# Performance work log

Hardware: AMD Instinct MI355X
Metric: run time of the kernel (lower is better)

Reference implementation:

```python
import jax, jax.numpy as jnp
import numpy as np

B, N, C = 1, 512, 64
CONTEXT = 3
HIDDEN = 256
N_OUT = 1
N_FEAT = C * 2 * CONTEXT  # join='cat' -> 2*C, then context shifts triple it
EPS = 1e-5


def pairing_cat(x_l, x_r, context):
    b, n, c = x_l.shape
    xl = jnp.broadcast_to(x_l[:, :, None, :], (b, n, n, c))
    xr = jnp.broadcast_to(x_r[:, None, :, :], (b, n, n, c))
    x = jnp.concatenate((xl, xr), axis=3)  # [B,N,N,2C]
    if context > 1:
        z = [x]
        for d in range(1, context // 2 + 1):
            z_u = jnp.zeros_like(x).at[:, d:, :-d, :].set(x[:, :-d, d:, :])
            z_d = jnp.zeros_like(x).at[:, :-d, d:, :].set(x[:, d:, :-d, :])
            z.append(z_u)
            z.append(z_d)
        x = jnp.concatenate(z, axis=3)  # [B,N,N,2C*context]
    return x


def setup_inputs() -> dict:
    key = jax.random.key(0)
    k = jax.random.split(key, 8)
    s1 = 1.0 / np.sqrt(N_FEAT)
    s2 = 1.0 / np.sqrt(HIDDEN)
    return {
        "x_l": jax.random.normal(k[0], (B, N, C), dtype=jnp.float32),
        "x_r": jax.random.normal(k[1], (B, N, C), dtype=jnp.float32),
        "W1": jax.random.uniform(k[2], (N_FEAT, HIDDEN), jnp.float32, -s1, s1),
        "b1": jax.random.uniform(k[3], (HIDDEN,), jnp.float32, -s1, s1),
        "gamma": jnp.ones((HIDDEN,), jnp.float32),
        "beta": jnp.zeros((HIDDEN,), jnp.float32),
        "W2": jax.random.uniform(k[4], (HIDDEN, N_OUT), jnp.float32, -s2, s2),
        "b2": jax.random.uniform(k[5], (N_OUT,), jnp.float32, -s2, s2),
    }


def reference(x_l, x_r, W1, b1, gamma, beta, W2, b2):
    x = pairing_cat(x_l, x_r, CONTEXT)  # [B,N,N,N_FEAT]
    h = jnp.einsum('bijf,fh->bijh', x, W1) + b1
    mu = jnp.mean(h, axis=-1, keepdims=True)
    var = jnp.mean(jnp.square(h - mu), axis=-1, keepdims=True)
    h = (h - mu) * jax.lax.rsqrt(var + EPS) * gamma + beta
    h = jax.nn.celu(h)  # dropout_rate=0.0 -> identity in eval/train
    y = jnp.einsum('bijh,ho->bijo', h, W2) + b2
    return y  # [B,N,N,1]
```

## Files before the change

### kernel.cpp

```cpp
#include <hip/hip_runtime.h>
#include <hip/hip_bf16.h>

#define NN  512
#define CC  64
#define HID 256
#define H4  (HID/4)
#define PSTRIDE (NN*HID)
#define PROWS 2

typedef short  bf16x8 __attribute__((ext_vector_type(8)));
typedef float  f32x4  __attribute__((ext_vector_type(4)));

__global__ __launch_bounds__(256) void proj_kernel(
    const float* __restrict__ xl, const float* __restrict__ xr,
    const float* __restrict__ W1, const float* __restrict__ b1,
    float* __restrict__ P)
{
  const int side = blockIdx.y;
  const int i0   = blockIdx.x * PROWS;
  const int h    = threadIdx.x;
  const float* __restrict__ x = side ? xr : xl;

  __shared__ float xs[PROWS][CC];
  if (threadIdx.x < PROWS * CC)
    xs[threadIdx.x >> 6][threadIdx.x & 63] = x[i0 * CC + threadIdx.x];
  __syncthreads();

  float acc0[PROWS], acc1[PROWS], acc2[PROWS];
#pragma unroll
  for (int r = 0; r < PROWS; r++) { acc0[r] = 0.f; acc1[r] = 0.f; acc2[r] = 0.f; }

  const int base = side ? CC : 0;
  const float* __restrict__ w0p = W1 + (base      ) * HID + h;
  const float* __restrict__ w1p = W1 + (base + 128) * HID + h;
  const float* __restrict__ w2p = W1 + (base + 256) * HID + h;
#pragma unroll 8
  for (int c = 0; c < CC; c++) {
    float w0 = w0p[c * HID];
    float w1 = w1p[c * HID];
    float w2 = w2p[c * HID];
#pragma unroll
    for (int r = 0; r < PROWS; r++) {
      float xv = xs[r][c];
      acc0[r] = fmaf(xv, w0, acc0[r]);
      acc1[r] = fmaf(xv, w1, acc1[r]);
      acc2[r] = fmaf(xv, w2, acc2[r]);
    }
  }

  float* __restrict__ O0 = P + (side ? 3 : 0) * PSTRIDE;
  float* __restrict__ O1 = P + (side ? 4 : 1) * PSTRIDE;
  float* __restrict__ O2 = P + (side ? 5 : 2) * PSTRIDE;
  const float bb = side ? 0.f : b1[h];
#pragma unroll
  for (int r = 0; r < PROWS; r++) {
    O0[(i0 + r) * HID + h] = acc0[r] + bb;
    O1[(i0 + r) * HID + h] = acc1[r];
    O2[(i0 + r) * HID + h] = acc2[r];
  }
}

__global__ __launch_bounds__(256) void prep_kernel(
    const float* __restrict__ P,
    float* __restrict__ Uf, float* __restrict__ Vf,
    unsigned short* __restrict__ Ubf, unsigned short* __restrict__ Vbf,
    float* __restrict__ rowstat)
{
  const int r = blockIdx.x, h = threadIdx.x;
  const float* __restrict__ PA = P;
  const float* __restrict__ PC = P + 1 * PSTRIDE;
  const float* __restrict__ PE = P + 2 * PSTRIDE;
  const float* __restrict__ PB = P + 3 * PSTRIDE;
  const float* __restrict__ PD = P + 4 * PSTRIDE;
  const float* __restrict__ PF = P + 5 * PSTRIDE;

  float u = PA[r * HID + h] + PC[(r - 1) * HID + h] + PE[(r + 1) * HID + h];
  float v = PB[r * HID + h] + PD[(r + 1) * HID + h] + PF[(r - 1) * HID + h];
  Uf[r * HID + h] = u;
  Vf[r * HID + h] = v;
  __hip_bfloat16 ub = __float2bfloat16(u), vb = __float2bfloat16(v);
  Ubf[r * HID + h] = *(unsigned short*)&ub;
  Vbf[r * HID + h] = *(unsigned short*)&vb;

  float u2 = u * u, v2 = v * v;
#pragma unroll
  for (int k = 32; k >= 1; k >>= 1) {
    u  += __shfl_xor(u,  k, 64);
    u2 += __shfl_xor(u2, k, 64);
    v  += __shfl_xor(v,  k, 64);
    v2 += __shfl_xor(v2, k, 64);
  }
  __shared__ float red[4][4];
  const int w = h >> 6;
  if ((h & 63) == 0) { red[w][0] = u; red[w][1] = u2; red[w][2] = v; red[w][3] = v2; }
  __syncthreads();
  if (h < 4)
    rowstat[h * NN + r] = red[0][h] + red[1][h] + red[2][h] + red[3][h];
}

__global__ __launch_bounds__(256) void cross_kernel(
    const unsigned short* __restrict__ Ubf,
    const unsigned short* __restrict__ Vbf,
    float* __restrict__ Cross)
{
  const int wave = threadIdx.x >> 6, lane = threadIdx.x & 63;
  const int t  = blockIdx.x * 4 + wave;
  const int ti = t >> 5, tj = t & 31;
  const int i0 = ti * 16, j0 = tj * 16;
  const int rc = lane & 15, kb = (lane >> 4) * 8;

  f32x4 acc = {0.f, 0.f, 0.f, 0.f};
#pragma unroll
  for (int k = 0; k < HID; k += 32) {
    bf16x8 a = *(const bf16x8*)(Ubf + (size_t)(i0 + rc) * HID + k + kb);
    bf16x8 b = *(const bf16x8*)(Vbf + (size_t)(j0 + rc) * HID + k + kb);
    acc = __builtin_amdgcn_mfma_f32_16x16x32_bf16(a, b, acc, 0, 0, 0);
  }
  const int orow = (lane >> 4) * 4, ocol = lane & 15;
#pragma unroll
  for (int r = 0; r < 4; r++)
    Cross[(size_t)(i0 + orow + r) * NN + j0 + ocol] = acc[r];
}

__device__ __forceinline__ float celu1(float x) {
  return fmaxf(x, 0.f) + fminf(__expf(x) - 1.f, 0.f);
}

__global__ __launch_bounds__(256) void pair_kernel(
    const float* __restrict__ P,
    const float* __restrict__ Uf, const float* __restrict__ Vf,
    const float* __restrict__ Cross, const float* __restrict__ rowstat,
    const float* __restrict__ gamma, const float* __restrict__ beta,
    const float* __restrict__ W2, const float* __restrict__ b2,
    float* __restrict__ out)
{
  const int wave = threadIdx.x >> 6, lane = threadIdx.x & 63;
  const float b2s = b2[0];

  if (blockIdx.x < 2040) {
    const int i     = 1 + (blockIdx.x >> 2);
    const int chunk = blockIdx.x & 3;
    const int g = lane >> 4, q = lane & 15;

    const float4* U4 = (const float4*)(Uf + i * HID + q * 16);
    const float4 u0 = U4[0], u1 = U4[1], u2 = U4[2], u3 = U4[3];
    const float4* G4 = (const float4*)(gamma + q * 16);
    const float4 ga0 = G4[0], ga1 = G4[1], ga2 = G4[2], ga3 = G4[3];
    const float4* B4 = (const float4*)(beta + q * 16);
    const float4 bt0 = B4[0], bt1 = B4[1], bt2 = B4[2], bt3 = B4[3];
    const float4* W4 = (const float4*)(W2 + q * 16);
    const float4 w0 = W4[0], w1 = W4[1], w2 = W4[2], w3 = W4[3];

    const float sUi  = rowstat[0 * NN + i];
    const float sU2i = rowstat[1 * NN + i];
    const float* __restrict__ sV  = rowstat + 2 * NN;
    const float* __restrict__ sV2 = rowstat + 3 * NN;

    const int jbase = 1 + chunk * 128 + wave * 32 + g;
    for (int m = 0; m < 8; m++) {
      const int j  = jbase + m * 4;
      const int jc = j <= 510 ? j : 510;
      const float4* V4 = (const float4*)(Vf + jc * HID + q * 16);
      const float4 v0 = V4[0], v1 = V4[1], v2 = V4[2], v3 = V4[3];
      const float Cr = Cross[i * NN + jc];
      const float mu = (sUi + sV[jc]) * (1.f / HID);
      const float t  = fmaf(2.f, Cr, sU2i + sV2[jc]) * (1.f / HID);
      const float rs = rsqrtf(t - mu * mu + 1e-5f);
      const float mrs = -mu * rs;

      float racc = 0.f;
      auto doh = [&](float U, float V, float G, float Bt, float W) {
        float s = U + V;
        float z = fmaf(s, rs, mrs);
        float n = fmaf(z, G, Bt);
        racc = fmaf(celu1(n), W, racc);
      };
      doh(u0.x, v0.x, ga0.x, bt0.x, w0.x);
      doh(u0.y, v0.y, ga0.y, bt0.y, w0.y);
      doh(u0.z, v0.z, ga0.z, bt0.z, w0.z);
      doh(u0.w, v0.w, ga0.w, bt0.w, w0.w);
      doh(u1.x, v1.x, ga1.x, bt1.x, w1.x);
      doh(u1.y, v1.y, ga1.y, bt1.y, w1.y);
      doh(u1.z, v1.z, ga1.z, bt1.z, w1.z);
      doh(u1.w, v1.w, ga1.w, bt1.w, w1.w);
      doh(u2.x, v2.x, ga2.x, bt2.x, w2.x);
      doh(u2.y, v2.y, ga2.y, bt2.y, w2.y);
      doh(u2.z, v2.z, ga2.z, bt2.z, w2.z);
      doh(u2.w, v2.w, ga2.w, bt2.w, w2.w);
      doh(u3.x, v3.x, ga3.x, bt3.x, w3.x);
      doh(u3.y, v3.y, ga3.y, bt3.y, w3.y);
      doh(u3.z, v3.z, ga3.z, bt3.z, w3.z);
      doh(u3.w, v3.w, ga3.w, bt3.w, w3.w);

#pragma unroll
      for (int k = 1; k <= 8; k <<= 1)
        racc += __shfl_xor(racc, k, 64);
      if (q == 0 && j <= 510)
        out[i * NN + j] = racc + b2s;
    }
  } else {
    const int gw = (blockIdx.x - 2040) * 4 + wave;
    const float4* P4 = (const float4*)P;
    const float4* PA = P4 + 0 * (PSTRIDE / 4);
    const float4* PC = P4 + 1 * (PSTRIDE / 4);
    const float4* PE = P4 + 2 * (PSTRIDE / 4);
    const float4* PB = P4 + 3 * (PSTRIDE / 4);
    const float4* PD = P4 + 4 * (PSTRIDE / 4);
    const float4* PF = P4 + 5 * (PSTRIDE / 4);
    const float4 g  = ((const float4*)gamma)[lane];
    const float4 be = ((const float4*)beta)[lane];
    const float4 w2 = ((const float4*)W2)[lane];

    for (int tt = 0; tt < 16; tt++) {
      const int p = gw * 16 + tt;
      if (p >= 2044) break;
      int i, j;
      if      (p < 512)  { i = 0;        j = p;        }
      else if (p < 1024) { i = 511;      j = p - 512;  }
      else if (p < 1534) { i = p - 1023; j = 0;        }
      else               { i = p - 1533; j = 511;      }

      const float4 a  = PA[i * H4 + lane];
      const float4 cu = PC[(i - 1) * H4 + lane];
      const float4 ed = PE[(i + 1) * H4 + lane];
      const float4 b  = PB[j * H4 + lane];
      const float4 du = PD[(j + 1) * H4 + lane];
      const float4 fd = PF[(j - 1) * H4 + lane];
      const float mu_m = (i >= 1 && j <= NN - 2) ? 1.f : 0.f;
      const float md_m = (i <= NN - 2 && j >= 1) ? 1.f : 0.f;

      float s0 = fmaf(md_m, ed.x + fd.x, fmaf(mu_m, cu.x + du.x, a.x + b.x));
      float s1 = fmaf(md_m, ed.y + fd.y, fmaf(mu_m, cu.y + du.y, a.y + b.y));
      float s2 = fmaf(md_m, ed.z + fd.z, fmaf(mu_m, cu.z + du.z, a.z + b.z));
      float s3 = fmaf(md_m, ed.w + fd.w, fmaf(mu_m, cu.w + du.w, a.w + b.w));

      float sum = (s0 + s1) + (s2 + s3);
      float ssq = fmaf(s0, s0, fmaf(s1, s1, fmaf(s2, s2, s3 * s3)));
#pragma unroll
      for (int off = 32; off >= 1; off >>= 1) {
        sum += __shfl_xor(sum, off, 64);
        ssq += __shfl_xor(ssq, off, 64);
      }
      const float mu  = sum * (1.f / HID);
      const float var = fmaf(ssq, 1.f / HID, -mu * mu);
      const float rs  = rsqrtf(var + 1e-5f);
      const float mrs = -mu * rs;

      auto nrm = [&](float s, float G, float Bt) {
        return fmaf(fmaf(s, rs, mrs), G, Bt);
      };
      float racc = fmaf(celu1(nrm(s0, g.x, be.x)), w2.x,
                   fmaf(celu1(nrm(s1, g.y, be.y)), w2.y,
                   fmaf(celu1(nrm(s2, g.z, be.z)), w2.z,
                        celu1(nrm(s3, g.w, be.w)) * w2.w)));
#pragma unroll
      for (int off = 32; off >= 1; off >>= 1)
        racc += __shfl_xor(racc, off, 64);
      if (lane == 0) out[i * NN + j] = racc + b2s;
    }
  }
}

extern "C" void kernel_launch(void* const* d_in, const int* in_sizes, int n_in,
                              void* d_out, int out_size, void* d_ws, size_t ws_size,
                              hipStream_t stream)
{
  const float* xl    = (const float*)d_in[0];
  const float* xr    = (const float*)d_in[1];
  const float* W1    = (const float*)d_in[2];
  const float* b1    = (const float*)d_in[3];
  const float* gamma = (const float*)d_in[4];
  const float* beta  = (const float*)d_in[5];
  const float* W2    = (const float*)d_in[6];
  const float* b2    = (const float*)d_in[7];
  float* out = (float*)d_out;

  float* P     = (float*)d_ws;
  float* Uf    = P + 6 * PSTRIDE;
  float* Vf    = Uf + NN * HID;
  float* Cross = Vf + NN * HID;
  unsigned short* Ubf = (unsigned short*)(Cross + NN * NN);
  unsigned short* Vbf = Ubf + NN * HID;
  float* rowstat = (float*)(Vbf + NN * HID);

  proj_kernel<<<dim3(NN / PROWS, 2), 256, 0, stream>>>(xl, xr, W1, b1, P);
  prep_kernel<<<NN, 256, 0, stream>>>(P, Uf, Vf, Ubf, Vbf, rowstat);
  cross_kernel<<<256, 256, 0, stream>>>(Ubf, Vbf, Cross);
  pair_kernel<<<2040 + 32, 256, 0, stream>>>(P, Uf, Vf, Cross, rowstat,
                                             gamma, beta, W2, b2, out);
}
```

Baseline: 124.5 us.

## Rebalance border work across more blocks, schedule first; split accumulators in pair kernel

The border-pair work moves from 32 trailing blocks of 16 pairs per wave to 256 leading blocks of 2 pairs per wave. This is meant to stop the slow border tail from running after the interior blocks finish. The interior loop now uses four independent accumulators to shorten the FMA dependency chain, simplifies CELU to a select, unrolls by 2, and adds an occupancy hint to launch bounds. The extra unrolling and the occupancy target may raise register pressure.

```diff
diff --git a/kernel.cpp b/kernel.cpp
--- a/kernel.cpp
+++ b/kernel.cpp
@@ -7,6 +7,7 @@
 #define H4  (HID/4)
 #define PSTRIDE (NN*HID)
 #define PROWS 2
+#define NB_BORDER 256
 
 typedef short  bf16x8 __attribute__((ext_vector_type(8)));
 typedef float  f32x4  __attribute__((ext_vector_type(4)));
@@ -123,10 +124,11 @@
 }
 
 __device__ __forceinline__ float celu1(float x) {
-  return fmaxf(x, 0.f) + fminf(__expf(x) - 1.f, 0.f);
-}
-
-__global__ __launch_bounds__(256) void pair_kernel(
+  float e = __expf(x) - 1.f;
+  return x > 0.f ? x : e;
+}
+
+__global__ __launch_bounds__(256, 6) void pair_kernel(
     const float* __restrict__ P,
     const float* __restrict__ Uf, const float* __restrict__ Vf,
     const float* __restrict__ Cross, const float* __restrict__ rowstat,
@@ -137,9 +139,10 @@
   const int wave = threadIdx.x >> 6, lane = threadIdx.x & 63;
   const float b2s = b2[0];
 
-  if (blockIdx.x < 2040) {
-    const int i     = 1 + (blockIdx.x >> 2);
-    const int chunk = blockIdx.x & 3;
+  if (blockIdx.x >= NB_BORDER) {
+    const int bx    = blockIdx.x - NB_BORDER;
+    const int i     = 1 + (bx >> 2);
+    const int chunk = bx & 3;
     const int g = lane >> 4, q = lane & 15;
 
     const float4* U4 = (const float4*)(Uf + i * HID + q * 16);
@@ -157,6 +160,7 @@
     const float* __restrict__ sV2 = rowstat + 3 * NN;
 
     const int jbase = 1 + chunk * 128 + wave * 32 + g;
+#pragma unroll 2
     for (int m = 0; m < 8; m++) {
       const int j  = jbase + m * 4;
       const int jc = j <= 510 ? j : 510;
@@ -168,29 +172,29 @@
       const float rs = rsqrtf(t - mu * mu + 1e-5f);
       const float mrs = -mu * rs;
 
-      float racc = 0.f;
-      auto doh = [&](float U, float V, float G, float Bt, float W) {
+      auto doh = [&](float& acc, float U, float V, float G, float Bt, float W) {
         float s = U + V;
-        float z = fmaf(s, rs, mrs);
-        float n = fmaf(z, G, Bt);
-        racc = fmaf(celu1(n), W, racc);
+        float n = fmaf(fmaf(s, rs, mrs), G, Bt);
+        acc = fmaf(celu1(n), W, acc);
       };
-      doh(u0.x, v0.x, ga0.x, bt0.x, w0.x);
-      doh(u0.y, v0.y, ga0.y, bt0.y, w0.y);
-      doh(u0.z, v0.z, ga0.z, bt0.z, w0.z);
-      doh(u0.w, v0.w, ga0.w, bt0.w, w0.w);
-      doh(u1.x, v1.x, ga1.x, bt1.x, w1.x);
-      doh(u1.y, v1.y, ga1.y, bt1.y, w1.y);
-      doh(u1.z, v1.z, ga1.z, bt1.z, w1.z);
-      doh(u1.w, v1.w, ga1.w, bt1.w, w1.w);
-      doh(u2.x, v2.x, ga2.x, bt2.x, w2.x);
-      doh(u2.y, v2.y, ga2.y, bt2.y, w2.y);
-      doh(u2.z, v2.z, ga2.z, bt2.z, w2.z);
-      doh(u2.w, v2.w, ga2.w, bt2.w, w2.w);
-      doh(u3.x, v3.x, ga3.x, bt3.x, w3.x);
-      doh(u3.y, v3.y, ga3.y, bt3.y, w3.y);
-      doh(u3.z, v3.z, ga3.z, bt3.z, w3.z);
-      doh(u3.w, v3.w, ga3.w, bt3.w, w3.w);
+      float r0 = 0.f, r1 = 0.f, r2 = 0.f, r3 = 0.f;
+      doh(r0, u0.x, v0.x, ga0.x, bt0.x, w0.x);
+      doh(r0, u0.y, v0.y, ga0.y, bt0.y, w0.y);
+      doh(r0, u0.z, v0.z, ga0.z, bt0.z, w0.z);
+      doh(r0, u0.w, v0.w, ga0.w, bt0.w, w0.w);
+      doh(r1, u1.x, v1.x, ga1.x, bt1.x, w1.x);
+      doh(r1, u1.y, v1.y, ga1.y, bt1.y, w1.y);
+      doh(r1, u1.z, v1.z, ga1.z, bt1.z, w1.z);
+      doh(r1, u1.w, v1.w, ga1.w, bt1.w, w1.w);
+      doh(r2, u2.x, v2.x, ga2.x, bt2.x, w2.x);
+      doh(r2, u2.y, v2.y, ga2.y, bt2.y, w2.y);
+      doh(r2, u2.z, v2.z, ga2.z, bt2.z, w2.z);
+      doh(r2, u2.w, v2.w, ga2.w, bt2.w, w2.w);
+      doh(r3, u3.x, v3.x, ga3.x, bt3.x, w3.x);
+      doh(r3, u3.y, v3.y, ga3.y, bt3.y, w3.y);
+      doh(r3, u3.z, v3.z, ga3.z, bt3.z, w3.z);
+      doh(r3, u3.w, v3.w, ga3.w, bt3.w, w3.w);
+      float racc = (r0 + r1) + (r2 + r3);
 
 #pragma unroll
       for (int k = 1; k <= 8; k <<= 1)
@@ -199,7 +203,7 @@
         out[i * NN + j] = racc + b2s;
     }
   } else {
-    const int gw = (blockIdx.x - 2040) * 4 + wave;
+    const int gw = blockIdx.x * 4 + wave;
     const float4* P4 = (const float4*)P;
     const float4* PA = P4 + 0 * (PSTRIDE / 4);
     const float4* PC = P4 + 1 * (PSTRIDE / 4);
@@ -211,8 +215,9 @@
     const float4 be = ((const float4*)beta)[lane];
     const float4 w2 = ((const float4*)W2)[lane];
 
-    for (int tt = 0; tt < 16; tt++) {
-      const int p = gw * 16 + tt;
+#pragma unroll
+    for (int tt = 0; tt < 2; tt++) {
+      const int p = gw * 2 + tt;
       if (p >= 2044) break;
       int i, j;
       if      (p < 512)  { i = 0;        j = p;        }
@@ -286,6 +291,6 @@
   proj_kernel<<<dim3(NN / PROWS, 2), 256, 0, stream>>>(xl, xr, W1, b1, P);
   prep_kernel<<<NN, 256, 0, stream>>>(P, Uf, Vf, Ubf, Vbf, rowstat);
   cross_kernel<<<256, 256, 0, stream>>>(Ubf, Vbf, Cross);
-  pair_kernel<<<2040 + 32, 256, 0, stream>>>(P, Uf, Vf, Cross, rowstat,
-                                             gamma, beta, W2, b2, out);
-}
+  pair_kernel<<<NB_BORDER + 2040, 256, 0, stream>>>(P, Uf, Vf, Cross, rowstat,
+                                                    gamma, beta, W2, b2, out);
+}
```

Result: slower. 147.7 us (+18.7%).
